# Optimization experiments

Hardware: AMD Instinct MI355X
Metric: run time of the kernel (lower is better)

The kernel has to match this reference:

```python
import jax, jax.numpy as jnp
import numpy as np

EPS = 1e-5      # numerical floor for degrees / std / attenuation
LEAK = 0.01     # LeakyReLU slope of mixing FCLayer
AVG_D = 3.3     # log(avg_degree + 1) from init_kwargs
BIG = 1e30      # masking constant for max/min aggregators


def setup_inputs() -> dict:
    key = jax.random.key(0)
    ks = jax.random.split(key, 12)
    B, N, Din, De, H = 8, 256, 128, 64, 128
    s = 0.05
    inp = {
        "input": jax.random.normal(ks[0], (B, N, Din), jnp.float32),
        "adj": (jax.random.uniform(ks[1], (B, N, N)) < 0.1).astype(jnp.float32),
        "adj_features": jax.random.normal(ks[2], (B, N, N, De), jnp.float32),
        "hidden": jnp.zeros((B * N, H), jnp.float32),
        "pre_W": jax.random.normal(ks[3], (2 * Din + De, Din), jnp.float32) * s,
        "pre_b": jnp.zeros((Din,), jnp.float32),
        "post_W": jax.random.normal(ks[4], (13 * Din, H), jnp.float32) * s,
        "post_b": jnp.zeros((H,), jnp.float32),
        "mix_W": jax.random.normal(ks[5], (H, H), jnp.float32) * s,
        "mix_b": jnp.zeros((H,), jnp.float32),
        "gru_Wih": jax.random.normal(ks[6], (3 * H, H), jnp.float32) * s,
        "gru_Whh": jax.random.normal(ks[7], (3 * H, H), jnp.float32) * s,
    }
    return inp


def reference(input, adj, adj_features, hidden, pre_W, pre_b, post_W, post_b,
              mix_W, mix_b, gru_Wih, gru_Whh):
    B, N, Din = input.shape
    H = mix_W.shape[1]
    # --- pretrans MLP over all pairs: Linear([h_i, h_j, e_ij]) ---
    # split the weight into blocks so we never materialize h_cat (B,N,N,2Din+De)
    Wi, Wj, We = pre_W[:Din], pre_W[Din:2 * Din], pre_W[2 * Din:]
    hi = input @ Wi            # (B,N,Din)
    hj = input @ Wj            # (B,N,Din)
    h_mod = (hi[:, :, None, :] + hj[:, None, :, :]
             + jnp.einsum('bije,ek->bijk', adj_features, We) + pre_b)  # (B,N,N,Din)
    # --- multi-aggregator masked reduction over source axis j ---
    deg = jnp.sum(adj, axis=2)                       # (B,N)
    degc = jnp.maximum(deg, EPS)[..., None]          # (B,N,1)
    s1 = jnp.einsum('bij,bijk->bik', adj, h_mod)
    s2 = jnp.einsum('bij,bijk->bik', adj, h_mod * h_mod)
    mean = s1 / degc
    var = jnp.maximum(s2 / degc - mean * mean, 0.0)
    std = jnp.sqrt(var + EPS)
    mask = adj[..., None] > 0
    has_nb = (deg > 0)[..., None]
    mx = jnp.where(has_nb, jnp.max(jnp.where(mask, h_mod, -BIG), axis=2), 0.0)
    mn = jnp.where(has_nb, jnp.min(jnp.where(mask, h_mod, BIG), axis=2), 0.0)
    m = jnp.concatenate([mean, mx, mn, std], axis=2)  # (B,N,4*Din)
    # --- scalers: identity, amplification, attenuation ---
    slog = (jnp.log(deg + 1.0) / AVG_D)[..., None]    # (B,N,1)
    m = jnp.concatenate([m, m * slog, m / (slog + EPS)], axis=2)  # (B,N,12*Din)
    # --- posttrans Linear + mixing FCLayer (LeakyReLU) ---
    m_cat = jnp.concatenate([input, m], axis=2)       # (B,N,13*Din)
    y = m_cat @ post_W + post_b                       # (B,N,H)
    y = y @ mix_W + mix_b
    y = jnp.where(y > 0, y, LEAK * y)
    # --- GRUCell (bias=False), torch gate order r,z,n ---
    x = y.reshape(B * N, H)
    gi = x @ gru_Wih.T
    gh = hidden @ gru_Whh.T
    r = jax.nn.sigmoid(gi[:, :H] + gh[:, :H])
    z = jax.nn.sigmoid(gi[:, H:2 * H] + gh[:, H:2 * H])
    n = jnp.tanh(gi[:, 2 * H:] + r * gh[:, 2 * H:])
    h_new = (1.0 - z) * n + z * hidden
    return h_new.reshape(B, N, H)
```

## Files before the change

kernel.cpp:

```cpp
#include <hip/hip_runtime.h>
#include <cstdint>
#include <cstddef>

#define EPSF 1e-5f
#define LEAKF 0.01f
#define AVGD 3.3f

static constexpr int Nn = 256, DIN = 128, DE = 64, Hn = 128;
static constexpr int BN = 2048;
static constexpr int CT = 1664;

typedef short bf16x8 __attribute__((ext_vector_type(8)));
typedef float f32x4  __attribute__((ext_vector_type(4)));
union BF8 { bf16x8 v; uint16_t u[8]; };

__device__ __forceinline__ float bf2f(uint16_t u) { return __uint_as_float(((uint32_t)u) << 16); }
__device__ __forceinline__ float bflo(uint32_t u)  { return __uint_as_float(u << 16); }
__device__ __forceinline__ uint16_t f2bf(float f) {
  uint32_t u = __float_as_uint(f);
  u += 0x7fffu + ((u >> 16) & 1u);
  return (uint16_t)(u >> 16);
}

__device__ __forceinline__ int detect_bf16(const uint32_t* w) {
  float lo = bflo(w[threadIdx.x & 63]);
  unsigned long long ok = __ballot(fabsf(lo) < 64.f);
  return ok == 0xFFFFFFFFFFFFFFFFull;
}
__device__ __forceinline__ float loadf(const void* p, size_t i, int isbf) {
  return isbf ? bf2f(((const uint16_t*)p)[i]) : ((const float*)p)[i];
}
__device__ __forceinline__ f32x4 mfma16(bf16x8 a, bf16x8 b, f32x4 c) {
  return __builtin_amdgcn_mfma_f32_16x16x32_bf16(a, b, c, 0, 0, 0);
}

__global__ __launch_bounds__(256) void k_prep(
    const void* __restrict__ input, const void* __restrict__ pre_W,
    const void* __restrict__ post_W, const void* __restrict__ mix_W,
    const void* __restrict__ Wih, const void* __restrict__ Whh,
    const void* __restrict__ hidden,
    uint16_t* __restrict__ preWb, uint16_t* __restrict__ postTb,
    uint16_t* __restrict__ mixTb, uint16_t* __restrict__ Wihb,
    uint16_t* __restrict__ Whhb, uint16_t* __restrict__ hidb,
    uint16_t* __restrict__ Ab) {
  int isbf = detect_bf16((const uint32_t*)input);
  int b = blockIdx.x, tid = threadIdx.x;
  if (b < 232) {
    if (b >= 16 && b < 24) return;
    __shared__ float tile[32][33];
    const void* src; int off, R, C, t; uint16_t* bdst;
    if (b < 16)      { src = mix_W;  off = 0; bdst = mixTb;  R = 128;  C = 128; t = b; }
    else             { src = post_W; off = 0; bdst = postTb; R = 1664; C = 128; t = b - 24; }
    int bx = t & 3, by = t >> 2;
    int tx = tid & 31, ty = tid >> 5;
    int c0 = bx * 32, r0 = by * 32;
    #pragma unroll
    for (int dy = 0; dy < 32; dy += 8) {
      size_t idx = (size_t)off + (size_t)(r0 + ty + dy) * C + (c0 + tx);
      tile[ty + dy][tx] = loadf(src, idx, isbf);
    }
    __syncthreads();
    #pragma unroll
    for (int dy = 0; dy < 32; dy += 8)
      bdst[(size_t)(c0 + ty + dy) * R + (r0 + tx)] = f2bf(tile[tx][ty + dy]);
  } else if (b < 428 && b >= 300) {
    int idx = (b - 300) * 2048 + tid * 8;
    int node = idx >> 7, col = idx & 127;
    uint16_t v[8];
    if (isbf) *(uint4*)v = *(const uint4*)((const uint16_t*)input + idx);
    else { const float* s = (const float*)input + idx;
           #pragma unroll
           for (int e = 0; e < 8; e++) v[e] = f2bf(s[e]); }
    *(uint4*)(Ab + (size_t)node * CT + col) = *(uint4*)v;
  } else {
    const void* src; uint16_t* dst; int base;
    if (b < 252)      { src = pre_W;  dst = preWb; base = (b - 232) * 2048; }
    else if (b < 276) { src = Wih;    dst = Wihb;  base = (b - 252) * 2048; }
    else if (b < 300) { src = Whh;    dst = Whhb;  base = (b - 276) * 2048; }
    else              { src = hidden; dst = hidb;  base = (b - 428) * 2048; }
    int i = base + tid * 8;
    uint16_t v[8];
    if (isbf) *(uint4*)v = *(const uint4*)((const uint16_t*)src + i);
    else { const float* s = (const float*)src + i;
           #pragma unroll
           for (int e = 0; e < 8; e++) v[e] = f2bf(s[e]); }
    *(uint4*)(dst + i) = *(uint4*)v;
  }
}

__global__ __launch_bounds__(256) void k1_mfma(
    const uint16_t* __restrict__ Ab, const uint16_t* __restrict__ preWb,
    const void* __restrict__ pre_b, const void* __restrict__ input_flag,
    float* __restrict__ hi, float* __restrict__ hj) {
  int isbf = detect_bf16((const uint32_t*)input_flag);
  int tid = threadIdx.x;
  int lane = tid & 63, w = tid >> 6;
  int wg = blockIdx.x * 4 + w;
  int rt = wg >> 4, nt = wg & 15;
  int ishj = nt >> 3, ct = nt & 7;
  int m16 = lane & 15, quad = lane >> 4;
  int col = ct * 16 + m16;
  const uint16_t* ap = Ab + (size_t)(rt * 16 + m16) * CT + quad * 8;
  int kbase = ishj ? 128 : 0;
  f32x4 acc = {0.f, 0.f, 0.f, 0.f};
  #pragma unroll
  for (int kt = 0; kt < 4; kt++) {
    bf16x8 a = *(const bf16x8*)(ap + kt * 32);
    BF8 bb;
    #pragma unroll
    for (int j = 0; j < 8; j++)
      bb.u[j] = preWb[(size_t)(kbase + kt * 32 + quad * 8 + j) * 128 + col];
    acc = mfma16(a, bb.v, acc);
  }
  float bias = ishj ? 0.f : loadf(pre_b, col, isbf);
  float* dst = ishj ? hj : hi;
  #pragma unroll
  for (int r = 0; r < 4; r++)
    dst[(size_t)(rt * 16 + quad * 4 + r) * 128 + col] = acc[r] + bias;
}

__global__ __launch_bounds__(256) void k2_mfma(
    const void* __restrict__ input, const void* __restrict__ adj_raw,
    const void* __restrict__ af_raw,
    const float* __restrict__ hi, const float* __restrict__ hj,
    const uint16_t* __restrict__ preWb, uint16_t* __restrict__ Ab) {
  __shared__ int s_cnt;
  __shared__ int nbr[Nn];
  __shared__ __align__(16) uint16_t A_lds[16 * 72];
  int isbf = detect_bf16((const uint32_t*)input);
  int bi = blockIdx.x, tid = threadIdx.x;
  if (tid == 0) s_cnt = 0;
  __syncthreads();
  {
    float a = loadf(adj_raw, (size_t)bi * Nn + tid, isbf);
    if (a > 0.f) nbr[atomicAdd(&s_cnt, 1)] = tid;
  }
  __syncthreads();
  int cnt = s_cnt;

  int lane = tid & 63, w = tid >> 6;
  int m16 = lane & 15, quad = lane >> 4;
  int col0 = w * 32 + m16, col1 = col0 + 16;

  BF8 b00, b01, b10, b11;
  #pragma unroll
  for (int j = 0; j < 8; j++) {
    int k0 = 256 + quad * 8 + j, k1 = k0 + 32;
    b00.u[j] = preWb[(size_t)k0 * 128 + col0];
    b01.u[j] = preWb[(size_t)k1 * 128 + col0];
    b10.u[j] = preWb[(size_t)k0 * 128 + col1];
    b11.u[j] = preWb[(size_t)k1 * 128 + col1];
  }
  float base0 = hi[(size_t)bi * 128 + col0];
  float base1 = hi[(size_t)bi * 128 + col1];
  const float* hjb = &hj[(size_t)(bi & ~(Nn - 1)) * 128];

  float s1a = 0.f, s2a = 0.f, mxa = -1e30f, mna = 1e30f;
  float s1b = 0.f, s2b = 0.f, mxb = -1e30f, mnb = 1e30f;

  for (int ce = 0; ce < cnt; ce += 16) {
    __syncthreads();
    if (tid < 128) {
      int e = tid >> 3, seg = tid & 7;
      int ei = ce + e; if (ei >= cnt) ei = cnt - 1;
      int j = nbr[ei];
      uint16_t v[8];
      if (isbf)
        *(uint4*)v = *(const uint4*)((const uint16_t*)af_raw + ((size_t)bi * Nn + j) * DE + seg * 8);
      else {
        const float* s = (const float*)af_raw + ((size_t)bi * Nn + j) * DE + seg * 8;
        #pragma unroll
        for (int x = 0; x < 8; x++) v[x] = f2bf(s[x]);
      }
      *(uint4*)&A_lds[e * 72 + seg * 8] = *(uint4*)v;
    }
    __syncthreads();
    float hjv0[4], hjv1[4]; int vld[4];
    #pragma unroll
    for (int r = 0; r < 4; r++) {
      int e = ce + quad * 4 + r;
      vld[r] = (e < cnt);
      int j = nbr[vld[r] ? e : (cnt - 1)];
      hjv0[r] = hjb[(size_t)j * 128 + col0];
      hjv1[r] = hjb[(size_t)j * 128 + col1];
    }
    bf16x8 a0 = *(const bf16x8*)&A_lds[m16 * 72 + quad * 8];
    bf16x8 a1 = *(const bf16x8*)&A_lds[m16 * 72 + 32 + quad * 8];
    f32x4 C0 = {0.f,0.f,0.f,0.f}, C1 = C0;
    C0 = mfma16(a0, b00.v, C0); C0 = mfma16(a1, b01.v, C0);
    C1 = mfma16(a0, b10.v, C1); C1 = mfma16(a1, b11.v, C1);
    #pragma unroll
    for (int r = 0; r < 4; r++) {
      float h0 = base0 + hjv0[r] + C0[r];
      float h1 = base1 + hjv1[r] + C1[r];
      if (vld[r]) {
        s1a += h0; s2a += h0 * h0; mxa = fmaxf(mxa, h0); mna = fminf(mna, h0);
        s1b += h1; s2b += h1 * h1; mxb = fmaxf(mxb, h1); mnb = fminf(mnb, h1);
      }
    }
  }
  #pragma unroll
  for (int off = 16; off <= 32; off <<= 1) {
    s1a += __shfl_xor(s1a, off); s2a += __shfl_xor(s2a, off);
    mxa = fmaxf(mxa, __shfl_xor(mxa, off)); mna = fminf(mna, __shfl_xor(mna, off));
    s1b += __shfl_xor(s1b, off); s2b += __shfl_xor(s2b, off);
    mxb = fmaxf(mxb, __shfl_xor(mxb, off)); mnb = fminf(mnb, __shfl_xor(mnb, off));
  }
  if (quad == 0) {
    float deg = (float)cnt, degc = fmaxf(deg, EPSF);
    float slog = logf(deg + 1.f) / AVGD;
    float inv  = 1.f / (slog + EPSF);
    uint16_t* mo = Ab + (size_t)bi * CT + 128;
    #pragma unroll
    for (int t = 0; t < 2; t++) {
      float s1 = t ? s1b : s1a, s2 = t ? s2b : s2a;
      float mx = t ? mxb : mxa, mn = t ? mnb : mna;
      int col = t ? col1 : col0;
      float mean = s1 / degc;
      float var  = fmaxf(s2 / degc - mean * mean, 0.f);
      float stdv = sqrtf(var + EPSF);
      if (cnt == 0) { mx = 0.f; mn = 0.f; }
      mo[0*128+col]  = f2bf(mean);        mo[1*128+col]  = f2bf(mx);
      mo[2*128+col]  = f2bf(mn);          mo[3*128+col]  = f2bf(stdv);
      mo[4*128+col]  = f2bf(mean * slog); mo[5*128+col]  = f2bf(mx * slog);
      mo[6*128+col]  = f2bf(mn * slog);   mo[7*128+col]  = f2bf(stdv * slog);
      mo[8*128+col]  = f2bf(mean * inv);  mo[9*128+col]  = f2bf(mx * inv);
      mo[10*128+col] = f2bf(mn * inv);    mo[11*128+col] = f2bf(stdv * inv);
    }
  }
}

__global__ __launch_bounds__(256) void k3a(
    const uint16_t* __restrict__ Ab, const uint16_t* __restrict__ postTb,
    const void* __restrict__ post_b, const void* __restrict__ input_flag,
    uint16_t* __restrict__ yb) {
  int isbf = detect_bf16((const uint32_t*)input_flag);
  int tid = threadIdx.x;
  int lane = tid & 63, w = tid >> 6;
  int wg = blockIdx.x * 4 + w;
  int rt = wg >> 3, ct = wg & 7;
  int m16 = lane & 15, quad = lane >> 4;
  const uint16_t* ap = Ab     + (size_t)(rt * 16 + m16) * CT + quad * 8;
  const uint16_t* bp = postTb + (size_t)(ct * 16 + m16) * CT + quad * 8;
  f32x4 acc0 = {0.f,0.f,0.f,0.f}, acc1 = acc0;
  #pragma unroll 4
  for (int kt = 0; kt < 52; kt += 2) {
    bf16x8 a0 = *(const bf16x8*)(ap + kt * 32);
    bf16x8 b0 = *(const bf16x8*)(bp + kt * 32);
    bf16x8 a1 = *(const bf16x8*)(ap + kt * 32 + 32);
    bf16x8 b1 = *(const bf16x8*)(bp + kt * 32 + 32);
    acc0 = mfma16(a0, b0, acc0);
    acc1 = mfma16(a1, b1, acc1);
  }
  int col = ct * 16 + m16;
  float pb = loadf(post_b, col, isbf);
  #pragma unroll
  for (int r = 0; r < 4; r++)
    yb[(size_t)(rt * 16 + quad * 4 + r) * 128 + col] = f2bf(acc0[r] + acc1[r] + pb);
}

__global__ __launch_bounds__(512) void k3b(
    const uint16_t* __restrict__ yb, const uint16_t* __restrict__ mixTb,
    const void* __restrict__ mix_b, const uint16_t* __restrict__ Wihb,
    const uint16_t* __restrict__ Whhb, const uint16_t* __restrict__ hidb,
    const void* __restrict__ input_flag, void* __restrict__ out) {
  constexpr int SX = 136;
  __shared__ __align__(16) uint16_t x_s[16 * SX];
  __shared__ __align__(16) uint16_t hid_s[16 * SX];
  int isbf = detect_bf16((const uint32_t*)input_flag);
  int tid = threadIdx.x;
  int n0 = blockIdx.x * 16;
  if (tid < 256) {
    int row = tid >> 4, c = (tid & 15) * 8;
    *(uint4*)&hid_s[row * SX + c] = *(const uint4*)&hidb[(size_t)(n0 + row) * 128 + c];
  }
  int lane = tid & 63, w = tid >> 6;
  int m16 = lane & 15, quad = lane >> 4;
  int col = w * 16 + m16;

  f32x4 acc = {0.f,0.f,0.f,0.f};
  const uint16_t* ya = yb    + (size_t)(n0 + m16) * 128 + quad * 8;
  const uint16_t* mb = mixTb + (size_t)col * 128 + quad * 8;
  #pragma unroll
  for (int kt = 0; kt < 4; kt++)
    acc = mfma16(*(const bf16x8*)(ya + kt * 32), *(const bf16x8*)(mb + kt * 32), acc);
  float mbias = loadf(mix_b, col, isbf);
  __syncthreads();
  #pragma unroll
  for (int r = 0; r < 4; r++) {
    float v = acc[r] + mbias; v = v > 0.f ? v : LEAKF * v;
    x_s[(quad * 4 + r) * SX + col] = f2bf(v);
  }
  __syncthreads();

  f32x4 gi[3], gh[3];
  #pragma unroll
  for (int q = 0; q < 3; q++) { gi[q] = {0.f,0.f,0.f,0.f}; gh[q] = {0.f,0.f,0.f,0.f}; }
  const uint16_t* xa = &x_s[m16 * SX + quad * 8];
  const uint16_t* ha = &hid_s[m16 * SX + quad * 8];
  #pragma unroll
  for (int kt = 0; kt < 4; kt++) {
    bf16x8 ax = *(const bf16x8*)(xa + kt * 32);
    bf16x8 ah = *(const bf16x8*)(ha + kt * 32);
    #pragma unroll
    for (int q = 0; q < 3; q++) {
      bf16x8 bi = *(const bf16x8*)&Wihb[(size_t)(q * 128 + col) * 128 + kt * 32 + quad * 8];
      bf16x8 bh = *(const bf16x8*)&Whhb[(size_t)(q * 128 + col) * 128 + kt * 32 + quad * 8];
      gi[q] = mfma16(ax, bi, gi[q]);
      gh[q] = mfma16(ah, bh, gh[q]);
    }
  }
  #pragma unroll
  for (int r = 0; r < 4; r++) {
    int row = quad * 4 + r;
    float rg = 1.f / (1.f + expf(-(gi[0][r] + gh[0][r])));
    float zg = 1.f / (1.f + expf(-(gi[1][r] + gh[1][r])));
    float ng = tanhf(gi[2][r] + rg * gh[2][r]);
    float hv = bf2f(hid_s[row * SX + col]);
    float res = (1.f - zg) * ng + zg * hv;
    size_t oi = (size_t)(n0 + row) * 128 + col;
    if (isbf) ((uint16_t*)out)[oi] = f2bf(res);
    else      ((float*)out)[oi]    = res;
  }
}

extern "C" void kernel_launch(void* const* d_in, const int* in_sizes, int n_in,
                              void* d_out, int out_size, void* d_ws, size_t ws_size,
                              hipStream_t stream) {
  const void* input  = d_in[0];
  const void* adj    = d_in[1];
  const void* af     = d_in[2];
  const void* hidden = d_in[3];
  const void* pre_W  = d_in[4];
  const void* pre_b  = d_in[5];
  const void* post_W = d_in[6];
  const void* post_b = d_in[7];
  const void* mix_W  = d_in[8];
  const void* mix_b  = d_in[9];
  const void* Wih    = d_in[10];
  const void* Whh    = d_in[11];

  float* ws = (float*)d_ws;
  float* hi = ws;
  float* hj = hi + 262144;
  uint16_t* Ab     = (uint16_t*)(hj + 262144);
  uint16_t* postTb = Ab + (size_t)BN * CT;
  uint16_t* mixTb  = postTb + 212992;
  uint16_t* preWb  = mixTb + 16384;
  uint16_t* Wihb   = preWb + 40960;
  uint16_t* Whhb   = Wihb + 49152;
  uint16_t* hidb   = Whhb + 49152;
  uint16_t* yb     = hidb + 262144;

  k_prep<<<556, 256, 0, stream>>>(input, pre_W, post_W, mix_W, Wih, Whh, hidden,
                                  preWb, postTb, mixTb, Wihb, Whhb, hidb, Ab);
  k1_mfma<<<512, 256, 0, stream>>>(Ab, preWb, pre_b, input, hi, hj);
  k2_mfma<<<BN, 256, 0, stream>>>(input, adj, af, hi, hj, preWb, Ab);
  k3a<<<256, 256, 0, stream>>>(Ab, postTb, post_b, input, yb);
  k3b<<<128, 512, 0, stream>>>(yb, mixTb, mix_b, Wihb, Whhb, hidb, input, d_out);
}
```

Measured before the change: 228.8 us.

## Fuse prep with hi/hj GEMM, double-buffer edge staging, merge post/mix/GRU kernels

Folds the hi/hj projection into the weight-prep kernel, which now reads raw input and pre_W directly, so one launch and the bf16 staging copies of input and hidden go away. k2 double-buffers the edge-feature LDS tile so the next chunk's gather overlaps the current MFMA work, and it drops one barrier per iteration. The post-transform GEMM is fused into the mix+GRU kernel, which keeps y in LDS instead of a global round-trip. The trade-off is that the fused k3 runs only 128 blocks, each doing the full K=1664 reduction per 16-row tile, which lowers parallelism for that GEMM.

New measurement: 238.1 us. +4.1%, slower.

```diff
diff --git a/kernel.cpp b/kernel.cpp
--- a/kernel.cpp
+++ b/kernel.cpp
@@ -8,7 +8,8 @@
 
 static constexpr int Nn = 256, DIN = 128, DE = 64, Hn = 128;
 static constexpr int BN = 2048;
-static constexpr int CT = 1664;
+static constexpr int KP = 1664;
+static constexpr int KM = 1536;
 
 typedef short bf16x8 __attribute__((ext_vector_type(8)));
 typedef float f32x4  __attribute__((ext_vector_type(4)));
@@ -30,103 +31,95 @@
 __device__ __forceinline__ float loadf(const void* p, size_t i, int isbf) {
   return isbf ? bf2f(((const uint16_t*)p)[i]) : ((const float*)p)[i];
 }
+__device__ __forceinline__ bf16x8 load_a8(const void* p, size_t elem, int isbf) {
+  if (isbf) return *(const bf16x8*)((const uint16_t*)p + elem);
+  const float* s = (const float*)p + elem;
+  BF8 r;
+  #pragma unroll
+  for (int e = 0; e < 8; e++) r.u[e] = f2bf(s[e]);
+  return r.v;
+}
 __device__ __forceinline__ f32x4 mfma16(bf16x8 a, bf16x8 b, f32x4 c) {
   return __builtin_amdgcn_mfma_f32_16x16x32_bf16(a, b, c, 0, 0, 0);
 }
 
-__global__ __launch_bounds__(256) void k_prep(
+__global__ __launch_bounds__(256) void k_prep1(
     const void* __restrict__ input, const void* __restrict__ pre_W,
-    const void* __restrict__ post_W, const void* __restrict__ mix_W,
-    const void* __restrict__ Wih, const void* __restrict__ Whh,
-    const void* __restrict__ hidden,
-    uint16_t* __restrict__ preWb, uint16_t* __restrict__ postTb,
-    uint16_t* __restrict__ mixTb, uint16_t* __restrict__ Wihb,
-    uint16_t* __restrict__ Whhb, uint16_t* __restrict__ hidb,
-    uint16_t* __restrict__ Ab) {
+    const void* __restrict__ pre_b, const void* __restrict__ post_W,
+    const void* __restrict__ mix_W, const void* __restrict__ Wih,
+    const void* __restrict__ Whh,
+    uint16_t* __restrict__ postTb, uint16_t* __restrict__ mixTb,
+    uint16_t* __restrict__ WeB, uint16_t* __restrict__ Wihb,
+    uint16_t* __restrict__ Whhb,
+    float* __restrict__ hi, float* __restrict__ hj) {
+  __shared__ float tile[32][33];
   int isbf = detect_bf16((const uint32_t*)input);
   int b = blockIdx.x, tid = threadIdx.x;
-  if (b < 232) {
-    if (b >= 16 && b < 24) return;
-    __shared__ float tile[32][33];
-    const void* src; int off, R, C, t; uint16_t* bdst;
-    if (b < 16)      { src = mix_W;  off = 0; bdst = mixTb;  R = 128;  C = 128; t = b; }
-    else             { src = post_W; off = 0; bdst = postTb; R = 1664; C = 128; t = b - 24; }
+
+  if (b >= 276) {
+    int lane = tid & 63, w = tid >> 6;
+    int wg = (b - 276) * 4 + w;
+    int rt = wg >> 4, nt = wg & 15;
+    int ishj = nt >> 3, ct = nt & 7;
+    int m16 = lane & 15, quad = lane >> 4;
+    int col = ct * 16 + m16;
+    int row = rt * 16 + m16;
+    int kbase = ishj ? 128 : 0;
+    f32x4 acc = {0.f, 0.f, 0.f, 0.f};
+    #pragma unroll
+    for (int kt = 0; kt < 4; kt++) {
+      bf16x8 a = load_a8(input, (size_t)row * 128 + kt * 32 + quad * 8, isbf);
+      BF8 bb;
+      #pragma unroll
+      for (int j = 0; j < 8; j++)
+        bb.u[j] = f2bf(loadf(pre_W, (size_t)(kbase + kt * 32 + quad * 8 + j) * 128 + col, isbf));
+      acc = mfma16(a, bb.v, acc);
+    }
+    float bias = ishj ? 0.f : loadf(pre_b, col, isbf);
+    float* dst = ishj ? hj : hi;
+    #pragma unroll
+    for (int r = 0; r < 4; r++)
+      dst[(size_t)(rt * 16 + quad * 4 + r) * 128 + col] = acc[r] + bias;
+    return;
+  }
+
+  if (b < 224) {
+    const void* src; uint16_t* bdst; int R, t;
+    if (b < 208) { src = post_W; bdst = postTb; R = KP;  t = b; }
+    else         { src = mix_W;  bdst = mixTb;  R = 128; t = b - 208; }
     int bx = t & 3, by = t >> 2;
     int tx = tid & 31, ty = tid >> 5;
     int c0 = bx * 32, r0 = by * 32;
     #pragma unroll
-    for (int dy = 0; dy < 32; dy += 8) {
-      size_t idx = (size_t)off + (size_t)(r0 + ty + dy) * C + (c0 + tx);
-      tile[ty + dy][tx] = loadf(src, idx, isbf);
-    }
+    for (int dy = 0; dy < 32; dy += 8)
+      tile[ty + dy][tx] = loadf(src, (size_t)(r0 + ty + dy) * 128 + (c0 + tx), isbf);
     __syncthreads();
     #pragma unroll
     for (int dy = 0; dy < 32; dy += 8)
       bdst[(size_t)(c0 + ty + dy) * R + (r0 + tx)] = f2bf(tile[tx][ty + dy]);
-  } else if (b < 428 && b >= 300) {
-    int idx = (b - 300) * 2048 + tid * 8;
-    int node = idx >> 7, col = idx & 127;
-    uint16_t v[8];
-    if (isbf) *(uint4*)v = *(const uint4*)((const uint16_t*)input + idx);
-    else { const float* s = (const float*)input + idx;
-           #pragma unroll
-           for (int e = 0; e < 8; e++) v[e] = f2bf(s[e]); }
-    *(uint4*)(Ab + (size_t)node * CT + col) = *(uint4*)v;
   } else {
-    const void* src; uint16_t* dst; int base;
-    if (b < 252)      { src = pre_W;  dst = preWb; base = (b - 232) * 2048; }
-    else if (b < 276) { src = Wih;    dst = Wihb;  base = (b - 252) * 2048; }
-    else if (b < 300) { src = Whh;    dst = Whhb;  base = (b - 276) * 2048; }
-    else              { src = hidden; dst = hidb;  base = (b - 428) * 2048; }
+    const void* src; uint16_t* dst; int base; size_t soff = 0;
+    if (b < 228)      { src = pre_W; dst = WeB;  base = (b - 224) * 2048; soff = 256 * 128; }
+    else if (b < 252) { src = Wih;   dst = Wihb; base = (b - 228) * 2048; }
+    else              { src = Whh;   dst = Whhb; base = (b - 252) * 2048; }
     int i = base + tid * 8;
     uint16_t v[8];
-    if (isbf) *(uint4*)v = *(const uint4*)((const uint16_t*)src + i);
-    else { const float* s = (const float*)src + i;
+    if (isbf) *(uint4*)v = *(const uint4*)((const uint16_t*)src + soff + i);
+    else { const float* s = (const float*)src + soff + i;
            #pragma unroll
            for (int e = 0; e < 8; e++) v[e] = f2bf(s[e]); }
     *(uint4*)(dst + i) = *(uint4*)v;
   }
-}
-
-__global__ __launch_bounds__(256) void k1_mfma(
-    const uint16_t* __restrict__ Ab, const uint16_t* __restrict__ preWb,
-    const void* __restrict__ pre_b, const void* __restrict__ input_flag,
-    float* __restrict__ hi, float* __restrict__ hj) {
-  int isbf = detect_bf16((const uint32_t*)input_flag);
-  int tid = threadIdx.x;
-  int lane = tid & 63, w = tid >> 6;
-  int wg = blockIdx.x * 4 + w;
-  int rt = wg >> 4, nt = wg & 15;
-  int ishj = nt >> 3, ct = nt & 7;
-  int m16 = lane & 15, quad = lane >> 4;
-  int col = ct * 16 + m16;
-  const uint16_t* ap = Ab + (size_t)(rt * 16 + m16) * CT + quad * 8;
-  int kbase = ishj ? 128 : 0;
-  f32x4 acc = {0.f, 0.f, 0.f, 0.f};
-  #pragma unroll
-  for (int kt = 0; kt < 4; kt++) {
-    bf16x8 a = *(const bf16x8*)(ap + kt * 32);
-    BF8 bb;
-    #pragma unroll
-    for (int j = 0; j < 8; j++)
-      bb.u[j] = preWb[(size_t)(kbase + kt * 32 + quad * 8 + j) * 128 + col];
-    acc = mfma16(a, bb.v, acc);
-  }
-  float bias = ishj ? 0.f : loadf(pre_b, col, isbf);
-  float* dst = ishj ? hj : hi;
-  #pragma unroll
-  for (int r = 0; r < 4; r++)
-    dst[(size_t)(rt * 16 + quad * 4 + r) * 128 + col] = acc[r] + bias;
 }
 
 __global__ __launch_bounds__(256) void k2_mfma(
     const void* __restrict__ input, const void* __restrict__ adj_raw,
     const void* __restrict__ af_raw,
     const float* __restrict__ hi, const float* __restrict__ hj,
-    const uint16_t* __restrict__ preWb, uint16_t* __restrict__ Ab) {
+    const uint16_t* __restrict__ WeB, uint16_t* __restrict__ Mb) {
   __shared__ int s_cnt;
   __shared__ int nbr[Nn];
-  __shared__ __align__(16) uint16_t A_lds[16 * 72];
+  __shared__ __align__(16) uint16_t A_lds[2][16 * 72];
   int isbf = detect_bf16((const uint32_t*)input);
   int bi = blockIdx.x, tid = threadIdx.x;
   if (tid == 0) s_cnt = 0;
@@ -145,11 +138,11 @@
   BF8 b00, b01, b10, b11;
   #pragma unroll
   for (int j = 0; j < 8; j++) {
-    int k0 = 256 + quad * 8 + j, k1 = k0 + 32;
-    b00.u[j] = preWb[(size_t)k0 * 128 + col0];
-    b01.u[j] = preWb[(size_t)k1 * 128 + col0];
-    b10.u[j] = preWb[(size_t)k0 * 128 + col1];
-    b11.u[j] = preWb[(size_t)k1 * 128 + col1];
+    int k0 = quad * 8 + j, k1 = k0 + 32;
+    b00.u[j] = WeB[(size_t)k0 * 128 + col0];
+    b01.u[j] = WeB[(size_t)k1 * 128 + col0];
+    b10.u[j] = WeB[(size_t)k0 * 128 + col1];
+    b11.u[j] = WeB[(size_t)k1 * 128 + col1];
   }
   float base0 = hi[(size_t)bi * 128 + col0];
   float base1 = hi[(size_t)bi * 128 + col1];
@@ -158,8 +151,7 @@
   float s1a = 0.f, s2a = 0.f, mxa = -1e30f, mna = 1e30f;
   float s1b = 0.f, s2b = 0.f, mxb = -1e30f, mnb = 1e30f;
 
-  for (int ce = 0; ce < cnt; ce += 16) {
-    __syncthreads();
+  auto stage = [&](int ce, int buf) {
     if (tid < 128) {
       int e = tid >> 3, seg = tid & 7;
       int ei = ce + e; if (ei >= cnt) ei = cnt - 1;
@@ -172,9 +164,16 @@
         #pragma unroll
         for (int x = 0; x < 8; x++) v[x] = f2bf(s[x]);
       }
-      *(uint4*)&A_lds[e * 72 + seg * 8] = *(uint4*)v;
-    }
-    __syncthreads();
+      *(uint4*)&A_lds[buf][e * 72 + seg * 8] = *(uint4*)v;
+    }
+  };
+
+  if (cnt > 0) stage(0, 0);
+  __syncthreads();
+
+  for (int ce = 0; ce < cnt; ce += 16) {
+    int cur = (ce >> 4) & 1;
+    if (ce + 16 < cnt) stage(ce + 16, cur ^ 1);
     float hjv0[4], hjv1[4]; int vld[4];
     #pragma unroll
     for (int r = 0; r < 4; r++) {
@@ -184,8 +183,8 @@
       hjv0[r] = hjb[(size_t)j * 128 + col0];
       hjv1[r] = hjb[(size_t)j * 128 + col1];
     }
-    bf16x8 a0 = *(const bf16x8*)&A_lds[m16 * 72 + quad * 8];
-    bf16x8 a1 = *(const bf16x8*)&A_lds[m16 * 72 + 32 + quad * 8];
+    bf16x8 a0 = *(const bf16x8*)&A_lds[cur][m16 * 72 + quad * 8];
+    bf16x8 a1 = *(const bf16x8*)&A_lds[cur][m16 * 72 + 32 + quad * 8];
     f32x4 C0 = {0.f,0.f,0.f,0.f}, C1 = C0;
     C0 = mfma16(a0, b00.v, C0); C0 = mfma16(a1, b01.v, C0);
     C1 = mfma16(a0, b10.v, C1); C1 = mfma16(a1, b11.v, C1);
@@ -198,7 +197,9 @@
         s1b += h1; s2b += h1 * h1; mxb = fmaxf(mxb, h1); mnb = fminf(mnb, h1);
       }
     }
-  }
+    __syncthreads();
+  }
+
   #pragma unroll
   for (int off = 16; off <= 32; off <<= 1) {
     s1a += __shfl_xor(s1a, off); s2a += __shfl_xor(s2a, off);
@@ -210,7 +211,7 @@
     float deg = (float)cnt, degc = fmaxf(deg, EPSF);
     float slog = logf(deg + 1.f) / AVGD;
     float inv  = 1.f / (slog + EPSF);
-    uint16_t* mo = Ab + (size_t)bi * CT + 128;
+    uint16_t* mo = Mb + (size_t)bi * KM;
     #pragma unroll
     for (int t = 0; t < 2; t++) {
       float s1 = t ? s1b : s1a, s2 = t ? s2b : s2a;
@@ -230,62 +231,63 @@
   }
 }
 
-__global__ __launch_bounds__(256) void k3a(
-    const uint16_t* __restrict__ Ab, const uint16_t* __restrict__ postTb,
-    const void* __restrict__ post_b, const void* __restrict__ input_flag,
-    uint16_t* __restrict__ yb) {
-  int isbf = detect_bf16((const uint32_t*)input_flag);
-  int tid = threadIdx.x;
-  int lane = tid & 63, w = tid >> 6;
-  int wg = blockIdx.x * 4 + w;
-  int rt = wg >> 3, ct = wg & 7;
-  int m16 = lane & 15, quad = lane >> 4;
-  const uint16_t* ap = Ab     + (size_t)(rt * 16 + m16) * CT + quad * 8;
-  const uint16_t* bp = postTb + (size_t)(ct * 16 + m16) * CT + quad * 8;
-  f32x4 acc0 = {0.f,0.f,0.f,0.f}, acc1 = acc0;
-  #pragma unroll 4
-  for (int kt = 0; kt < 52; kt += 2) {
-    bf16x8 a0 = *(const bf16x8*)(ap + kt * 32);
-    bf16x8 b0 = *(const bf16x8*)(bp + kt * 32);
-    bf16x8 a1 = *(const bf16x8*)(ap + kt * 32 + 32);
-    bf16x8 b1 = *(const bf16x8*)(bp + kt * 32 + 32);
-    acc0 = mfma16(a0, b0, acc0);
-    acc1 = mfma16(a1, b1, acc1);
-  }
-  int col = ct * 16 + m16;
-  float pb = loadf(post_b, col, isbf);
-  #pragma unroll
-  for (int r = 0; r < 4; r++)
-    yb[(size_t)(rt * 16 + quad * 4 + r) * 128 + col] = f2bf(acc0[r] + acc1[r] + pb);
-}
-
-__global__ __launch_bounds__(512) void k3b(
-    const uint16_t* __restrict__ yb, const uint16_t* __restrict__ mixTb,
-    const void* __restrict__ mix_b, const uint16_t* __restrict__ Wihb,
-    const uint16_t* __restrict__ Whhb, const uint16_t* __restrict__ hidb,
-    const void* __restrict__ input_flag, void* __restrict__ out) {
+__global__ __launch_bounds__(512) void k3_fused(
+    const void* __restrict__ input, const uint16_t* __restrict__ Mb,
+    const uint16_t* __restrict__ postTb, const void* __restrict__ post_b,
+    const uint16_t* __restrict__ mixTb, const void* __restrict__ mix_b,
+    const uint16_t* __restrict__ Wihb, const uint16_t* __restrict__ Whhb,
+    const void* __restrict__ hidden, void* __restrict__ out) {
   constexpr int SX = 136;
+  __shared__ __align__(16) uint16_t y_s[16 * SX];
   __shared__ __align__(16) uint16_t x_s[16 * SX];
   __shared__ __align__(16) uint16_t hid_s[16 * SX];
-  int isbf = detect_bf16((const uint32_t*)input_flag);
+  int isbf = detect_bf16((const uint32_t*)input);
   int tid = threadIdx.x;
   int n0 = blockIdx.x * 16;
   if (tid < 256) {
     int row = tid >> 4, c = (tid & 15) * 8;
-    *(uint4*)&hid_s[row * SX + c] = *(const uint4*)&hidb[(size_t)(n0 + row) * 128 + c];
+    uint16_t v[8];
+    if (isbf) *(uint4*)v = *(const uint4*)((const uint16_t*)hidden + (size_t)(n0 + row) * 128 + c);
+    else { const float* s = (const float*)hidden + (size_t)(n0 + row) * 128 + c;
+           #pragma unroll
+           for (int e = 0; e < 8; e++) v[e] = f2bf(s[e]); }
+    *(uint4*)&hid_s[row * SX + c] = *(uint4*)v;
   }
   int lane = tid & 63, w = tid >> 6;
   int m16 = lane & 15, quad = lane >> 4;
   int col = w * 16 + m16;
 
+  f32x4 acc0 = {0.f,0.f,0.f,0.f}, acc1 = acc0;
+  const uint16_t* bp = postTb + (size_t)col * KP + quad * 8;
+  #pragma unroll
+  for (int kt = 0; kt < 4; kt += 2) {
+    bf16x8 a0 = load_a8(input, (size_t)(n0 + m16) * 128 + kt * 32 + quad * 8, isbf);
+    bf16x8 a1 = load_a8(input, (size_t)(n0 + m16) * 128 + kt * 32 + 32 + quad * 8, isbf);
+    acc0 = mfma16(a0, *(const bf16x8*)(bp + kt * 32), acc0);
+    acc1 = mfma16(a1, *(const bf16x8*)(bp + kt * 32 + 32), acc1);
+  }
+  const uint16_t* mp  = Mb + (size_t)(n0 + m16) * KM + quad * 8;
+  const uint16_t* bp2 = bp + 4 * 32;
+  #pragma unroll 4
+  for (int kt = 0; kt < 48; kt += 2) {
+    bf16x8 a0 = *(const bf16x8*)(mp + kt * 32);
+    bf16x8 a1 = *(const bf16x8*)(mp + kt * 32 + 32);
+    acc0 = mfma16(a0, *(const bf16x8*)(bp2 + kt * 32), acc0);
+    acc1 = mfma16(a1, *(const bf16x8*)(bp2 + kt * 32 + 32), acc1);
+  }
+  float pb = loadf(post_b, col, isbf);
+  #pragma unroll
+  for (int r = 0; r < 4; r++)
+    y_s[(quad * 4 + r) * SX + col] = f2bf(acc0[r] + acc1[r] + pb);
+  __syncthreads();
+
   f32x4 acc = {0.f,0.f,0.f,0.f};
-  const uint16_t* ya = yb    + (size_t)(n0 + m16) * 128 + quad * 8;
+  const uint16_t* ya = &y_s[m16 * SX + quad * 8];
   const uint16_t* mb = mixTb + (size_t)col * 128 + quad * 8;
   #pragma unroll
   for (int kt = 0; kt < 4; kt++)
     acc = mfma16(*(const bf16x8*)(ya + kt * 32), *(const bf16x8*)(mb + kt * 32), acc);
   float mbias = loadf(mix_b, col, isbf);
-  __syncthreads();
   #pragma unroll
   for (int r = 0; r < 4; r++) {
     float v = acc[r] + mbias; v = v > 0.f ? v : LEAKF * v;
@@ -304,10 +306,10 @@
     bf16x8 ah = *(const bf16x8*)(ha + kt * 32);
     #pragma unroll
     for (int q = 0; q < 3; q++) {
-      bf16x8 bi = *(const bf16x8*)&Wihb[(size_t)(q * 128 + col) * 128 + kt * 32 + quad * 8];
-      bf16x8 bh = *(const bf16x8*)&Whhb[(size_t)(q * 128 + col) * 128 + kt * 32 + quad * 8];
-      gi[q] = mfma16(ax, bi, gi[q]);
-      gh[q] = mfma16(ah, bh, gh[q]);
+      bf16x8 bi_ = *(const bf16x8*)&Wihb[(size_t)(q * 128 + col) * 128 + kt * 32 + quad * 8];
+      bf16x8 bh_ = *(const bf16x8*)&Whhb[(size_t)(q * 128 + col) * 128 + kt * 32 + quad * 8];
+      gi[q] = mfma16(ax, bi_, gi[q]);
+      gh[q] = mfma16(ah, bh_, gh[q]);
     }
   }
   #pragma unroll
@@ -343,19 +345,16 @@
   float* ws = (float*)d_ws;
   float* hi = ws;
   float* hj = hi + 262144;
-  uint16_t* Ab     = (uint16_t*)(hj + 262144);
-  uint16_t* postTb = Ab + (size_t)BN * CT;
+  uint16_t* postTb = (uint16_t*)(hj + 262144);
   uint16_t* mixTb  = postTb + 212992;
-  uint16_t* preWb  = mixTb + 16384;
-  uint16_t* Wihb   = preWb + 40960;
+  uint16_t* WeB    = mixTb + 16384;
+  uint16_t* Wihb   = WeB + 8192;
   uint16_t* Whhb   = Wihb + 49152;
-  uint16_t* hidb   = Whhb + 49152;
-  uint16_t* yb     = hidb + 262144;
-
-  k_prep<<<556, 256, 0, stream>>>(input, pre_W, post_W, mix_W, Wih, Whh, hidden,
-                                  preWb, postTb, mixTb, Wihb, Whhb, hidb, Ab);
-  k1_mfma<<<512, 256, 0, stream>>>(Ab, preWb, pre_b, input, hi, hj);
-  k2_mfma<<<BN, 256, 0, stream>>>(input, adj, af, hi, hj, preWb, Ab);
-  k3a<<<256, 256, 0, stream>>>(Ab, postTb, post_b, input, yb);
-  k3b<<<128, 512, 0, stream>>>(yb, mixTb, mix_b, Wihb, Whhb, hidb, input, d_out);
-}
+  uint16_t* Mb     = Whhb + 49152;
+
+  k_prep1<<<788, 256, 0, stream>>>(input, pre_W, pre_b, post_W, mix_W, Wih, Whh,
+                                   postTb, mixTb, WeB, Wihb, Whhb, hi, hj);
+  k2_mfma<<<BN, 256, 0, stream>>>(input, adj, af, hi, hj, WeB, Mb);
+  k3_fused<<<128, 512, 0, stream>>>(input, Mb, postTb, post_b, mixTb, mix_b,
+                                    Wihb, Whhb, hidden, d_out);
+}
```
